# Performance work log

Measured on AMD Instinct MI355X. Metric: run time of the kernel, lower is better.

The kernel has to match this reference:

```python
import jax, jax.numpy as jnp
import numpy as np

B, S, E, H = 2, 2048, 1024, 16
DH = E // H            # 64 head dim
ROT = DH // 2          # 32: RotaryEmbedding(head_dim//2) rotates first 32 dims only
CTX = 2048             # sliding KV window
THETA = 10000.0


def setup_inputs() -> dict:
    key = jax.random.key(0)
    ks = jax.random.split(key, 7)
    sc = 1.0 / np.sqrt(E)
    mk = lambda k, sh, s=1.0: (jax.random.normal(k, sh, jnp.float32) * s)
    return {
        "query": mk(ks[0], (B, S, E)),
        "key":   mk(ks[1], (B, S, E)),
        "value": mk(ks[2], (B, S, E)),
        "Wq": mk(ks[3], (E, E), sc), "bq": jnp.zeros((E,), jnp.float32),
        "Wk": mk(ks[4], (E, E), sc), "bk": jnp.zeros((E,), jnp.float32),
        "Wv": mk(ks[5], (E, E), sc), "bv": jnp.zeros((E,), jnp.float32),
        "Wo": mk(ks[6], (E, E), sc), "bo": jnp.zeros((E,), jnp.float32),
    }


def _rope(t):
    # t: [B, H, S, DH]; rotate first ROT dims, pass the rest through (offset=0).
    seq = t.shape[2]
    inv_freq = 1.0 / (THETA ** (jnp.arange(0, ROT, 2, dtype=jnp.float32) / ROT))  # [ROT//2]
    ang = jnp.arange(seq, dtype=jnp.float32)[:, None] * inv_freq[None, :]          # [S, ROT//2]
    cos = jnp.repeat(jnp.cos(ang), 2, axis=-1)  # [S, ROT] (pairwise-interleaved freqs)
    sin = jnp.repeat(jnp.sin(ang), 2, axis=-1)
    rot, rest = t[..., :ROT], t[..., ROT:]
    x1, x2 = rot[..., 0::2], rot[..., 1::2]
    rot_half = jnp.stack([-x2, x1], axis=-1).reshape(rot.shape)  # rotate_half on pairs
    return jnp.concatenate([rot * cos + rot_half * sin, rest], axis=-1)


def reference(query, key, value, Wq, bq, Wk, bk, Wv, bv, Wo, bo):
    def heads(x, W, b):
        return (x @ W.T + b).reshape(B, -1, H, DH).transpose(0, 2, 1, 3)  # [B,H,S,DH]

    q = _rope(heads(query, Wq, bq))
    k = _rope(heads(key, Wk, bk))
    v = heads(value, Wv, bv)
    k, v = k[:, :, -CTX:], v[:, :, -CTX:]  # sliding window (no-op when S == CTX)

    scale = jnp.float32(1.0 / np.sqrt(DH))
    scores = jnp.einsum('bhqd,bhkd->bhqk', q, k) * scale  # [B,H,Sq,Sk]
    sq, sk = q.shape[2], k.shape[2]
    causal = jnp.tril(jnp.ones((sk, sk), dtype=bool))[-sq:]  # [Sq,Sk]
    scores = jnp.where(causal[None, None], scores, jnp.float32(-jnp.inf))
    probs = jax.nn.softmax(scores, axis=-1)  # dropout=0 (eval)
    out = jnp.einsum('bhqk,bhkd->bhqd', probs, v)
    out = out.transpose(0, 2, 1, 3).reshape(B, -1, E)
    return out @ Wo.T + bo
```

## Files before the change

kernel.cpp:

```cpp
#include <hip/hip_runtime.h>
#include <stdint.h>
#include <math.h>

typedef __bf16 bf16x8 __attribute__((ext_vector_type(8)));
typedef float f32x4 __attribute__((ext_vector_type(4)));

__device__ __forceinline__ float bf2f(uint16_t x) {
  unsigned u = ((unsigned)x) << 16;
  float f;
  __builtin_memcpy(&f, &u, 4);
  return f;
}
__device__ __forceinline__ uint16_t f2bf(float f) {
  __bf16 h = (__bf16)f;
  uint16_t u;
  __builtin_memcpy(&u, &h, 2);
  return u;
}
__device__ __forceinline__ bf16x8 cvt8(const float* p) {
  const float4 lo = *(const float4*)p;
  const float4 hi = *(const float4*)(p + 4);
  bf16x8 v;
  v[0] = (__bf16)lo.x; v[1] = (__bf16)lo.y; v[2] = (__bf16)lo.z; v[3] = (__bf16)lo.w;
  v[4] = (__bf16)hi.x; v[5] = (__bf16)hi.y; v[6] = (__bf16)hi.z; v[7] = (__bf16)hi.w;
  return v;
}

typedef __attribute__((address_space(1))) const unsigned int gu32;
typedef __attribute__((address_space(3))) unsigned int lu32;
__device__ __forceinline__ void async_copy16(const void* gp, void* lp) {
  __builtin_amdgcn_global_load_lds((gu32*)gp, (lu32*)lp, 16, 0, 0);
}

__global__ __launch_bounds__(256) void cvt_kernel(
    const float* __restrict__ s0, uint16_t* __restrict__ d0,
    const float* __restrict__ s1, uint16_t* __restrict__ d1,
    const float* __restrict__ s2, uint16_t* __restrict__ d2) {
  const int z = blockIdx.z;
  const float* s = z == 0 ? s0 : z == 1 ? s1 : s2;
  uint16_t* d = z == 0 ? d0 : z == 1 ? d1 : d2;
  const size_t idx = ((size_t)blockIdx.x * 256 + threadIdx.x) * 8;
  *(bf16x8*)(d + idx) = cvt8(s + idx);
}

template <bool A_F32, bool W_F32, bool C_F32, bool VT, bool ROPE, int BM, int NF>
__global__ __launch_bounds__(256) void gemm3_kernel(
    const void* __restrict__ A0, const void* __restrict__ W0,
    const float* __restrict__ b0, void* __restrict__ C0,
    const void* __restrict__ A1, const void* __restrict__ W1,
    const float* __restrict__ b1, void* __restrict__ C1,
    const void* __restrict__ A2, const void* __restrict__ W2,
    const float* __restrict__ b2, void* __restrict__ C2,
    int M, int N, int K) {
  constexpr int BN = NF * 32;
  constexpr int AF = BM / 32;
  const int z = blockIdx.z;
  const void* Av = z == 0 ? A0 : z == 1 ? A1 : A2;
  const void* Wp = z == 0 ? W0 : z == 1 ? W1 : W2;
  const float* bias = z == 0 ? b0 : z == 1 ? b1 : b2;
  void* Cv = z == 0 ? C0 : z == 1 ? C1 : C2;

  __shared__ __align__(16) uint16_t As[BM * 64];
  __shared__ __align__(16) uint16_t Bs[BN * 64];
  const int tid = threadIdx.x;
  const int wave = tid >> 6, lane = tid & 63;
  const int quad = lane >> 4, l16 = lane & 15;
  const int l = blockIdx.y * gridDim.x + blockIdx.x;
  const int nmt = M / BM;
  const int bm = (l % nmt) * BM;
  const int bn = (l / nmt) * BN;
  const int wm = (wave >> 1) * (BM / 2);
  const int wn = (wave & 1) * (BN / 2);

  f32x4 acc[AF][NF] = {};

  for (int k0 = 0; k0 < K; k0 += 64) {
    bf16x8 ar[AF], wr[NF];
    if (A_F32) {
#pragma unroll
      for (int i = 0; i < AF; i++) {
        const int c = i * 256 + tid;
        const int r = c >> 3, pc = ((c & 7) ^ (r & 7)) << 3;
        ar[i] = cvt8((const float*)Av + (size_t)(bm + r) * K + k0 + pc);
      }
    }
    if (W_F32) {
#pragma unroll
      for (int i = 0; i < NF; i++) {
        const int c = i * 256 + tid;
        const int r = c >> 3, pc = ((c & 7) ^ (r & 7)) << 3;
        wr[i] = cvt8((const float*)Wp + (size_t)(bn + r) * K + k0 + pc);
      }
    }
    if (k0) __syncthreads();
#pragma unroll
    for (int i = 0; i < AF; i++) {
      const int c = i * 256 + tid;
      const int r = c >> 3, pc = ((c & 7) ^ (r & 7)) << 3;
      if (A_F32) *(bf16x8*)(As + c * 8) = ar[i];
      else async_copy16((const uint16_t*)Av + (size_t)(bm + r) * K + k0 + pc,
                        As + (i * 256 + (tid & 192)) * 8);
    }
#pragma unroll
    for (int i = 0; i < NF; i++) {
      const int c = i * 256 + tid;
      const int r = c >> 3, pc = ((c & 7) ^ (r & 7)) << 3;
      if (W_F32) *(bf16x8*)(Bs + c * 8) = wr[i];
      else async_copy16((const uint16_t*)Wp + (size_t)(bn + r) * K + k0 + pc,
                        Bs + (i * 256 + (tid & 192)) * 8);
    }
    __syncthreads();
#pragma unroll
    for (int s = 0; s < 2; s++) {
      bf16x8 af[AF], bfr[NF];
#pragma unroll
      for (int i = 0; i < AF; i++) {
        const int Ra = wm + i * 16 + l16;
        af[i] = *(const bf16x8*)(As + Ra * 64 + (((s * 4 + quad) ^ (Ra & 7)) << 3));
      }
#pragma unroll
      for (int j = 0; j < NF; j++) {
        const int Rb = wn + j * 16 + l16;
        bfr[j] = *(const bf16x8*)(Bs + Rb * 64 + (((s * 4 + quad) ^ (Rb & 7)) << 3));
      }
#pragma unroll
      for (int i = 0; i < AF; i++)
#pragma unroll
        for (int j = 0; j < NF; j++)
          acc[i][j] = __builtin_amdgcn_mfma_f32_16x16x32_bf16(af[i], bfr[j], acc[i][j], 0, 0, 0);
    }
  }
  if (VT && z == 2) {
#pragma unroll
    for (int j = 0; j < NF; j++) {
      const int n = bn + wn + j * 16 + l16;
      const float bj = bias[n];
      const int h = n >> 6, dh = n & 63;
#pragma unroll
      for (int i = 0; i < AF; i++) {
        const int m0 = bm + wm + i * 16 + quad * 4;
        const int b = m0 >> 11, s0 = m0 & 2047;
        uint2 pk;
        pk.x = (unsigned)f2bf(acc[i][j][0] + bj) |
               ((unsigned)f2bf(acc[i][j][1] + bj) << 16);
        pk.y = (unsigned)f2bf(acc[i][j][2] + bj) |
               ((unsigned)f2bf(acc[i][j][3] + bj) << 16);
        *(uint2*)((uint16_t*)Cv + ((size_t)((b * 16 + h) * 64 + dh)) * 2048 + s0) = pk;
      }
    }
  } else {
#pragma unroll
    for (int j = 0; j < NF; j++) {
      const int n = bn + wn + j * 16 + l16;
      const float bj = bias[n];
      const int dh = (wn + j * 16 + l16) & 63;
      const bool rot = ROPE && (((wn + j * 16) & 63) < 32);
      float invrev = 0.f;
      if (rot)
        invrev = __expf(-0.5756462732485115f * (float)(dh >> 1)) *
                 0.15915494309189535f;
#pragma unroll
      for (int i = 0; i < AF; i++) {
        const int m0 = bm + wm + i * 16 + quad * 4;
#pragma unroll
        for (int r = 0; r < 4; r++) {
          float v = acc[i][j][r] + bj;
          if (rot) {
            const int s_pos = (m0 + r) & 2047;
            float rev = (float)s_pos * invrev;
            rev -= floorf(rev);
            const float sn = __builtin_amdgcn_sinf(rev);
            const float cs = __builtin_amdgcn_cosf(rev);
            const float partner = __shfl_xor(v, 1);
            v = (dh & 1) ? (v * cs + partner * sn) : (v * cs - partner * sn);
          }
          if (C_F32) ((float*)Cv)[(size_t)(m0 + r) * N + n] = v;
          else       ((uint16_t*)Cv)[(size_t)(m0 + r) * N + n] = f2bf(v);
        }
      }
    }
  }
}

__global__ __launch_bounds__(256) void flash_kernel(const uint16_t* __restrict__ Q,
                                                    const uint16_t* __restrict__ K,
                                                    const uint16_t* __restrict__ VT,
                                                    uint16_t* __restrict__ AO) {
  const int bx = blockIdx.x;
  const int xcd = bx & 7;
  const int slot = bx >> 3;
  const int bh = (slot >> 4) * 8 + xcd;
  const int qt2 = 15 - (slot & 15);
  const int h = bh & 15;
  const int b = bh >> 4;
  const int tid = threadIdx.x;
  const int wave = tid >> 6, lane = tid & 63;
  const int quad = lane >> 4, l16 = lane & 15;

  __shared__ __align__(16) uint16_t Ks[64 * 64];
  __shared__ __align__(16) uint16_t Vt[64 * 64];
  __shared__ __align__(16) uint16_t Ps[4][32 * 72];

  const int qrow0 = qt2 * 128 + wave * 16 + l16;
  const int qrow1 = qrow0 + 64;
  bf16x8 qf0[2], qf1[2];
#pragma unroll
  for (int s = 0; s < 2; s++) {
    union { bf16x8 v; uint16_t u[8]; } t0, t1;
    t0.v = *(const bf16x8*)(Q + ((size_t)(b * 2048 + qrow0) * 1024) + h * 64 + s * 32 + quad * 8);
    t1.v = *(const bf16x8*)(Q + ((size_t)(b * 2048 + qrow1) * 1024) + h * 64 + s * 32 + quad * 8);
#pragma unroll
    for (int j = 0; j < 8; j++) {
      t0.u[j] = f2bf(bf2f(t0.u[j]) * 0.125f);
      t1.u[j] = f2bf(bf2f(t1.u[j]) * 0.125f);
    }
    qf0[s] = t0.v;
    qf1[s] = t1.v;
  }

  const size_t vbase = ((size_t)((b * 16 + h) * 64)) * 2048;

  float lsum0 = 0.f, lsum1 = 0.f;
  f32x4 o0[4] = {}, o1[4] = {};

  const int nkt = 2 * qt2 + 2;
  for (int kt = 0; kt < nkt; kt++) {
    if (kt) __syncthreads();
#pragma unroll
    for (int i = 0; i < 2; i++) {
      const int c = i * 256 + tid;
      const int r = c >> 3, pc = ((c & 7) ^ (r & 7)) << 3;
      async_copy16(K + ((size_t)(b * 2048 + kt * 64 + r) * 1024) + h * 64 + pc,
                   Ks + (i * 256 + (tid & 192)) * 8);
      async_copy16(VT + vbase + (size_t)r * 2048 + kt * 64 + pc,
                   Vt + (i * 256 + (tid & 192)) * 8);
    }
    __syncthreads();

    const bool f0 = (kt < nkt - 1);

    {
      f32x4 sacc[4] = {};
#pragma unroll
      for (int s = 0; s < 2; s++)
#pragma unroll
        for (int t = 0; t < 4; t++) {
          const int R = t * 16 + l16;
          bf16x8 kf = *(const bf16x8*)(Ks + R * 64 + (((s * 4 + quad) ^ (R & 7)) << 3));
          sacc[t] = __builtin_amdgcn_mfma_f32_16x16x32_bf16(kf, qf1[s], sacc[t], 0, 0, 0);
        }
      if (kt == nkt - 1) {
#pragma unroll
        for (int t = 0; t < 4; t++)
#pragma unroll
          for (int r = 0; r < 4; r++)
            if (kt * 64 + t * 16 + quad * 4 + r > qrow1) sacc[t][r] = -1e30f;
      }
#pragma unroll
      for (int t = 0; t < 4; t++) {
        float p0 = __expf(sacc[t][0]), p1 = __expf(sacc[t][1]);
        float p2 = __expf(sacc[t][2]), p3 = __expf(sacc[t][3]);
        lsum1 += (p0 + p1) + (p2 + p3);
        uint2 pk;
        pk.x = (unsigned)f2bf(p0) | ((unsigned)f2bf(p1) << 16);
        pk.y = (unsigned)f2bf(p2) | ((unsigned)f2bf(p3) << 16);
        *(uint2*)(&Ps[wave][(16 + l16) * 72 + t * 16 + quad * 4]) = pk;
      }
    }
    if (f0) {
      f32x4 sacc[4] = {};
#pragma unroll
      for (int s = 0; s < 2; s++)
#pragma unroll
        for (int t = 0; t < 4; t++) {
          const int R = t * 16 + l16;
          bf16x8 kf = *(const bf16x8*)(Ks + R * 64 + (((s * 4 + quad) ^ (R & 7)) << 3));
          sacc[t] = __builtin_amdgcn_mfma_f32_16x16x32_bf16(kf, qf0[s], sacc[t], 0, 0, 0);
        }
      if (kt == nkt - 2) {
#pragma unroll
        for (int t = 0; t < 4; t++)
#pragma unroll
          for (int r = 0; r < 4; r++)
            if (kt * 64 + t * 16 + quad * 4 + r > qrow0) sacc[t][r] = -1e30f;
      }
#pragma unroll
      for (int t = 0; t < 4; t++) {
        float p0 = __expf(sacc[t][0]), p1 = __expf(sacc[t][1]);
        float p2 = __expf(sacc[t][2]), p3 = __expf(sacc[t][3]);
        lsum0 += (p0 + p1) + (p2 + p3);
        uint2 pk;
        pk.x = (unsigned)f2bf(p0) | ((unsigned)f2bf(p1) << 16);
        pk.y = (unsigned)f2bf(p2) | ((unsigned)f2bf(p3) << 16);
        *(uint2*)(&Ps[wave][l16 * 72 + t * 16 + quad * 4]) = pk;
      }
    }
#pragma unroll
    for (int s = 0; s < 2; s++) {
      const bf16x8 pa1 = *(const bf16x8*)(&Ps[wave][(16 + l16) * 72 + s * 32 + quad * 8]);
#pragma unroll
      for (int t = 0; t < 4; t++) {
        const int R = t * 16 + l16;
        const bf16x8 vb = *(const bf16x8*)(Vt + R * 64 + (((s * 4 + quad) ^ (R & 7)) << 3));
        o1[t] = __builtin_amdgcn_mfma_f32_16x16x32_bf16(pa1, vb, o1[t], 0, 0, 0);
      }
    }
    if (f0) {
#pragma unroll
      for (int s = 0; s < 2; s++) {
        const bf16x8 pa0 = *(const bf16x8*)(&Ps[wave][l16 * 72 + s * 32 + quad * 8]);
#pragma unroll
        for (int t = 0; t < 4; t++) {
          const int R = t * 16 + l16;
          const bf16x8 vb = *(const bf16x8*)(Vt + R * 64 + (((s * 4 + quad) ^ (R & 7)) << 3));
          o0[t] = __builtin_amdgcn_mfma_f32_16x16x32_bf16(pa0, vb, o0[t], 0, 0, 0);
        }
      }
    }
  }
  lsum0 += __shfl_xor(lsum0, 16);
  lsum0 += __shfl_xor(lsum0, 32);
  lsum1 += __shfl_xor(lsum1, 16);
  lsum1 += __shfl_xor(lsum1, 32);
  const float inv0 = 1.f / lsum0, inv1 = 1.f / lsum1;
  float invr0[4], invr1[4];
#pragma unroll
  for (int r = 0; r < 4; r++) {
    invr0[r] = __shfl(inv0, quad * 4 + r);
    invr1[r] = __shfl(inv1, quad * 4 + r);
  }
#pragma unroll
  for (int t = 0; t < 4; t++)
#pragma unroll
    for (int r = 0; r < 4; r++) {
      const int qg0 = qt2 * 128 + wave * 16 + quad * 4 + r;
      AO[((size_t)(b * 2048 + qg0) * 1024) + h * 64 + t * 16 + l16] =
          f2bf(o0[t][r] * invr0[r]);
      AO[((size_t)(b * 2048 + qg0 + 64) * 1024) + h * 64 + t * 16 + l16] =
          f2bf(o1[t][r] * invr1[r]);
    }
}

extern "C" void kernel_launch(void* const* d_in, const int* in_sizes, int n_in,
                              void* d_out, int out_size, void* d_ws, size_t ws_size,
                              hipStream_t stream) {
  const float* query = (const float*)d_in[0];
  const float* key   = (const float*)d_in[1];
  const float* value = (const float*)d_in[2];
  const float* Wq = (const float*)d_in[3];
  const float* bq = (const float*)d_in[4];
  const float* Wk = (const float*)d_in[5];
  const float* bk = (const float*)d_in[6];
  const float* Wv = (const float*)d_in[7];
  const float* bv = (const float*)d_in[8];
  const float* Wo = (const float*)d_in[9];
  const float* bo = (const float*)d_in[10];
  float* out = (float*)d_out;

  uint16_t* ws = (uint16_t*)d_ws;
  uint16_t* Qb  = ws;
  uint16_t* Kb  = ws + (size_t)4194304;
  uint16_t* VTb = ws + (size_t)8388608;
  uint16_t* AOb = ws + (size_t)12582912;
  uint16_t* Wqc = AOb;
  uint16_t* Wkc = AOb + (size_t)1048576;
  uint16_t* Wvc = AOb + (size_t)2097152;

  dim3 blk(256);
  cvt_kernel<<<dim3(512, 1, 3), blk, 0, stream>>>(Wq, Wqc, Wk, Wkc, Wv, Wvc);
  gemm3_kernel<true, false, false, true, true, 128, 2><<<dim3(16, 32, 3), blk, 0, stream>>>(
      query, Wqc, bq, Qb,
      key,   Wkc, bk, Kb,
      value, Wvc, bv, VTb,
      4096, 1024, 1024);
  flash_kernel<<<dim3(512), blk, 0, stream>>>(Qb, Kb, VTb, AOb);
  gemm3_kernel<false, true, true, false, false, 64, 2><<<dim3(16, 64, 1), blk, 0, stream>>>(
      AOb, Wo, bo, out,
      AOb, Wo, bo, out,
      AOb, Wo, bo, out,
      4096, 1024, 1024);
}
```

Measured before the change: 254.2 us.

## Stage fp32 activations into LDS via async copies and convert at fragment load

The QKV projection GEMM now copies fp32 activation tiles straight into shared memory with asynchronous global-to-LDS loads instead of loading into registers and converting to bf16 before the store. The bf16 conversion moves to the point where MFMA fragments are read from LDS, using an XOR swizzle over 16-byte float groups. The A tile in LDS doubles in size for this path. Tile shapes also change: the QKV GEMM widens N per block (NF 2 to 4) and the output GEMM uses BM 128, which reduces grid size and raises per-block register and LDS use.

```diff
diff --git a/kernel.cpp b/kernel.cpp
--- a/kernel.cpp
+++ b/kernel.cpp
@@ -17,13 +17,14 @@
   __builtin_memcpy(&u, &h, 2);
   return u;
 }
-__device__ __forceinline__ bf16x8 cvt8(const float* p) {
-  const float4 lo = *(const float4*)p;
-  const float4 hi = *(const float4*)(p + 4);
+__device__ __forceinline__ bf16x8 pack8(float4 lo, float4 hi) {
   bf16x8 v;
   v[0] = (__bf16)lo.x; v[1] = (__bf16)lo.y; v[2] = (__bf16)lo.z; v[3] = (__bf16)lo.w;
   v[4] = (__bf16)hi.x; v[5] = (__bf16)hi.y; v[6] = (__bf16)hi.z; v[7] = (__bf16)hi.w;
   return v;
+}
+__device__ __forceinline__ bf16x8 cvt8(const float* p) {
+  return pack8(*(const float4*)p, *(const float4*)(p + 4));
 }
 
 typedef __attribute__((address_space(1))) const unsigned int gu32;
@@ -60,7 +61,7 @@
   const float* bias = z == 0 ? b0 : z == 1 ? b1 : b2;
   void* Cv = z == 0 ? C0 : z == 1 ? C1 : C2;
 
-  __shared__ __align__(16) uint16_t As[BM * 64];
+  __shared__ __align__(16) uint16_t As[BM * (A_F32 ? 128 : 64)];
   __shared__ __align__(16) uint16_t Bs[BN * 64];
   const int tid = threadIdx.x;
   const int wave = tid >> 6, lane = tid & 63;
@@ -75,15 +76,7 @@
   f32x4 acc[AF][NF] = {};
 
   for (int k0 = 0; k0 < K; k0 += 64) {
-    bf16x8 ar[AF], wr[NF];
-    if (A_F32) {
-#pragma unroll
-      for (int i = 0; i < AF; i++) {
-        const int c = i * 256 + tid;
-        const int r = c >> 3, pc = ((c & 7) ^ (r & 7)) << 3;
-        ar[i] = cvt8((const float*)Av + (size_t)(bm + r) * K + k0 + pc);
-      }
-    }
+    bf16x8 wr[NF];
     if (W_F32) {
 #pragma unroll
       for (int i = 0; i < NF; i++) {
@@ -93,13 +86,22 @@
       }
     }
     if (k0) __syncthreads();
-#pragma unroll
-    for (int i = 0; i < AF; i++) {
-      const int c = i * 256 + tid;
-      const int r = c >> 3, pc = ((c & 7) ^ (r & 7)) << 3;
-      if (A_F32) *(bf16x8*)(As + c * 8) = ar[i];
-      else async_copy16((const uint16_t*)Av + (size_t)(bm + r) * K + k0 + pc,
-                        As + (i * 256 + (tid & 192)) * 8);
+    if (A_F32) {
+#pragma unroll
+      for (int i = 0; i < BM / 16; i++) {
+        const int U = i * 256 + tid;
+        const int r = U >> 4, ug = (U & 15) ^ (r & 7);
+        async_copy16((const float*)Av + (size_t)(bm + r) * K + k0 + ug * 4,
+                     As + (i * 256 + (tid & 192)) * 8);
+      }
+    } else {
+#pragma unroll
+      for (int i = 0; i < AF; i++) {
+        const int c = i * 256 + tid;
+        const int r = c >> 3, pc = ((c & 7) ^ (r & 7)) << 3;
+        async_copy16((const uint16_t*)Av + (size_t)(bm + r) * K + k0 + pc,
+                     As + (i * 256 + (tid & 192)) * 8);
+      }
     }
 #pragma unroll
     for (int i = 0; i < NF; i++) {
@@ -116,7 +118,15 @@
 #pragma unroll
       for (int i = 0; i < AF; i++) {
         const int Ra = wm + i * 16 + l16;
-        af[i] = *(const bf16x8*)(As + Ra * 64 + (((s * 4 + quad) ^ (Ra & 7)) << 3));
+        if (A_F32) {
+          const float* Asf = (const float*)As;
+          const int g = ((s * 4 + quad) * 2) ^ (Ra & 7);
+          const float4 lo = *(const float4*)(Asf + Ra * 64 + g * 4);
+          const float4 hi = *(const float4*)(Asf + Ra * 64 + (g ^ 1) * 4);
+          af[i] = pack8(lo, hi);
+        } else {
+          af[i] = *(const bf16x8*)(As + Ra * 64 + (((s * 4 + quad) ^ (Ra & 7)) << 3));
+        }
       }
 #pragma unroll
       for (int j = 0; j < NF; j++) {
@@ -368,13 +378,13 @@
 
   dim3 blk(256);
   cvt_kernel<<<dim3(512, 1, 3), blk, 0, stream>>>(Wq, Wqc, Wk, Wkc, Wv, Wvc);
-  gemm3_kernel<true, false, false, true, true, 128, 2><<<dim3(16, 32, 3), blk, 0, stream>>>(
+  gemm3_kernel<true, false, false, true, true, 128, 4><<<dim3(8, 32, 3), blk, 0, stream>>>(
       query, Wqc, bq, Qb,
       key,   Wkc, bk, Kb,
       value, Wvc, bv, VTb,
       4096, 1024, 1024);
   flash_kernel<<<dim3(512), blk, 0, stream>>>(Qb, Kb, VTb, AOb);
-  gemm3_kernel<false, true, true, false, false, 64, 2><<<dim3(16, 64, 1), blk, 0, stream>>>(
+  gemm3_kernel<false, true, true, false, false, 128, 2><<<dim3(16, 32, 1), blk, 0, stream>>>(
       AOb, Wo, bo, out,
       AOb, Wo, bo, out,
       AOb, Wo, bo, out,
```

Result: faster. 243.0 us (-4.4%).

## Pre-convert activations and Wo to bf16, widen QKV GEMM tiles

Applied to the files above, without the earlier changes.

When the workspace is large enough, the inputs query/key/value and Wo are converted to bf16 in separate pre-pass kernels. The GEMMs can then stage bf16 operands asynchronously instead of converting fp32 on the fly. The QKV projection tile width is doubled (NF 2 to 4) and the output projection uses BM=128. This adds an extra pass over the activations and more workspace, in exchange for simpler, faster GEMM loads. A fallback path keeps the old scheme, also with the larger output tile.

```diff
diff --git a/kernel.cpp b/kernel.cpp
--- a/kernel.cpp
+++ b/kernel.cpp
@@ -17,14 +17,15 @@
   __builtin_memcpy(&u, &h, 2);
   return u;
 }
-__device__ __forceinline__ bf16x8 cvt8(const float* p) {
-  const float4 lo = *(const float4*)p;
-  const float4 hi = *(const float4*)(p + 4);
+__device__ __forceinline__ bf16x8 pack8(float4 lo, float4 hi) {
   bf16x8 v;
   v[0] = (__bf16)lo.x; v[1] = (__bf16)lo.y; v[2] = (__bf16)lo.z; v[3] = (__bf16)lo.w;
   v[4] = (__bf16)hi.x; v[5] = (__bf16)hi.y; v[6] = (__bf16)hi.z; v[7] = (__bf16)hi.w;
   return v;
 }
+__device__ __forceinline__ bf16x8 cvt8(const float* p) {
+  return pack8(*(const float4*)p, *(const float4*)(p + 4));
+}
 
 typedef __attribute__((address_space(1))) const unsigned int gu32;
 typedef __attribute__((address_space(3))) unsigned int lu32;
@@ -35,10 +36,11 @@
 __global__ __launch_bounds__(256) void cvt_kernel(
     const float* __restrict__ s0, uint16_t* __restrict__ d0,
     const float* __restrict__ s1, uint16_t* __restrict__ d1,
-    const float* __restrict__ s2, uint16_t* __restrict__ d2) {
+    const float* __restrict__ s2, uint16_t* __restrict__ d2,
+    const float* __restrict__ s3, uint16_t* __restrict__ d3) {
   const int z = blockIdx.z;
-  const float* s = z == 0 ? s0 : z == 1 ? s1 : s2;
-  uint16_t* d = z == 0 ? d0 : z == 1 ? d1 : d2;
+  const float* s = z == 0 ? s0 : z == 1 ? s1 : z == 2 ? s2 : s3;
+  uint16_t* d = z == 0 ? d0 : z == 1 ? d1 : z == 2 ? d2 : d3;
   const size_t idx = ((size_t)blockIdx.x * 256 + threadIdx.x) * 8;
   *(bf16x8*)(d + idx) = cvt8(s + idx);
 }
@@ -362,21 +364,49 @@
   uint16_t* Kb  = ws + (size_t)4194304;
   uint16_t* VTb = ws + (size_t)8388608;
   uint16_t* AOb = ws + (size_t)12582912;
-  uint16_t* Wqc = AOb;
-  uint16_t* Wkc = AOb + (size_t)1048576;
-  uint16_t* Wvc = AOb + (size_t)2097152;
 
   dim3 blk(256);
-  cvt_kernel<<<dim3(512, 1, 3), blk, 0, stream>>>(Wq, Wqc, Wk, Wkc, Wv, Wvc);
-  gemm3_kernel<true, false, false, true, true, 128, 2><<<dim3(16, 32, 3), blk, 0, stream>>>(
-      query, Wqc, bq, Qb,
-      key,   Wkc, bk, Kb,
-      value, Wvc, bv, VTb,
-      4096, 1024, 1024);
-  flash_kernel<<<dim3(512), blk, 0, stream>>>(Qb, Kb, VTb, AOb);
-  gemm3_kernel<false, true, true, false, false, 64, 2><<<dim3(16, 64, 1), blk, 0, stream>>>(
-      AOb, Wo, bo, out,
-      AOb, Wo, bo, out,
-      AOb, Wo, bo, out,
-      4096, 1024, 1024);
-}
+
+  if (ws_size >= (size_t)64 * 1024 * 1024) {
+    uint16_t* Qc  = ws + (size_t)16777216;
+    uint16_t* Kc  = ws + (size_t)20971520;
+    uint16_t* Vc  = ws + (size_t)25165824;
+    uint16_t* Wqc = ws + (size_t)29360128;
+    uint16_t* Wkc = ws + (size_t)30408704;
+    uint16_t* Wvc = ws + (size_t)31457280;
+    uint16_t* Woc = ws + (size_t)32505856;
+
+    cvt_kernel<<<dim3(512, 1, 4), blk, 0, stream>>>(
+        Wq, Wqc, Wk, Wkc, Wv, Wvc, Wo, Woc);
+    cvt_kernel<<<dim3(2048, 1, 3), blk, 0, stream>>>(
+        query, Qc, key, Kc, value, Vc, nullptr, nullptr);
+    gemm3_kernel<false, false, false, true, true, 128, 4><<<dim3(8, 32, 3), blk, 0, stream>>>(
+        Qc, Wqc, bq, Qb,
+        Kc, Wkc, bk, Kb,
+        Vc, Wvc, bv, VTb,
+        4096, 1024, 1024);
+    flash_kernel<<<dim3(512), blk, 0, stream>>>(Qb, Kb, VTb, AOb);
+    gemm3_kernel<false, false, true, false, false, 128, 2><<<dim3(16, 32, 1), blk, 0, stream>>>(
+        AOb, Woc, bo, out,
+        AOb, Woc, bo, out,
+        AOb, Woc, bo, out,
+        4096, 1024, 1024);
+  } else {
+    uint16_t* Wqc = AOb;
+    uint16_t* Wkc = AOb + (size_t)1048576;
+    uint16_t* Wvc = AOb + (size_t)2097152;
+    cvt_kernel<<<dim3(512, 1, 3), blk, 0, stream>>>(
+        Wq, Wqc, Wk, Wkc, Wv, Wvc, nullptr, nullptr);
+    gemm3_kernel<true, false, false, true, true, 128, 2><<<dim3(16, 32, 3), blk, 0, stream>>>(
+        query, Wqc, bq, Qb,
+        key,   Wkc, bk, Kb,
+        value, Wvc, bv, VTb,
+        4096, 1024, 1024);
+    flash_kernel<<<dim3(512), blk, 0, stream>>>(Qb, Kb, VTb, AOb);
+    gemm3_kernel<false, true, true, false, false, 128, 2><<<dim3(16, 32, 1), blk, 0, stream>>>(
+        AOb, Wo, bo, out,
+        AOb, Wo, bo, out,
+        AOb, Wo, bo, out,
+        4096, 1024, 1024);
+  }
+}
```

Result: faster. 230.0 us (-9.5%).
